# Performance work log

Hardware: AMD Instinct MI355X
Metric: run time of the kernel (lower is better)

The kernel has to match this reference:

```python
import jax, jax.numpy as jnp
import numpy as np

N, E, DIN, D, FE, L, B, M = 10000, 40000, 11, 64, 4, 4, 512, 3


def setup_inputs() -> dict:
    key = jax.random.key(0)
    ks = iter(jax.random.split(key, 24))
    s = lambda *sh: jax.random.normal(next(ks), sh, jnp.float32)
    return {
        "x": s(N, DIN),
        "edge_index": jax.random.randint(next(ks), (2, E), 0, N),
        "edge_attr": jax.random.uniform(next(ks), (E, FE), jnp.float32),
        "batch": jnp.sort(jax.random.randint(next(ks), (N,), 0, B)),
        "W0": s(DIN, D) * 0.1, "b0": jnp.zeros((D,), jnp.float32),
        "Wn1": s(FE, 2 * D) * 0.1, "bn1": jnp.zeros((2 * D,), jnp.float32),
        "Wn2": s(2 * D, D * D) * 0.02, "bn2": jnp.zeros((D * D,), jnp.float32),
        "root": s(L, D, D) * 0.1, "conv_bias": jnp.zeros((L, D), jnp.float32),
        "lstm_Wih": s(4 * D, 2 * D) * 0.1, "lstm_Whh": s(4 * D, D) * 0.1,
        "lstm_b": jnp.zeros((4 * D,), jnp.float32),
        "Wo1": s(2 * D, D) * 0.1, "bo1": jnp.zeros((D,), jnp.float32),
        "Wo2": s(D, 1) * 0.1, "bo2": jnp.zeros((1,), jnp.float32),
    }


def reference(x, edge_index, edge_attr, batch, W0, b0, Wn1, bn1, Wn2, bn2,
              root, conv_bias, lstm_Wih, lstm_Whh, lstm_b, Wo1, bo1, Wo2, bo2):
    src, dst = edge_index[0], edge_index[1]
    h = x @ W0 + b0  # [N, D]
    # Edge MLP is SHARED across all conv layers -> compute per-edge weight matrices once
    ew = (jax.nn.silu(edge_attr @ Wn1 + bn1) @ Wn2 + bn2).reshape(E, D, D)
    for l in range(L):
        msg = jnp.einsum('ed,edf->ef', h[src], ew)  # gather-compute per edge
        aggr = jax.ops.segment_sum(msg, dst, num_segments=N)  # scatter-add to targets
        h = h + (aggr + h @ root[l] + conv_bias[l])  # NNConv + residual
    # Set2Set pooling (LSTM, M processing steps)
    q_star = jnp.zeros((B, 2 * D), h.dtype)
    hs = jnp.zeros((B, D), h.dtype)
    cs = jnp.zeros((B, D), h.dtype)
    for _ in range(M):
        gates = q_star @ lstm_Wih.T + hs @ lstm_Whh.T + lstm_b
        i, f, g, o = jnp.split(gates, 4, axis=-1)  # torch LSTM gate order
        cs = jax.nn.sigmoid(f) * cs + jax.nn.sigmoid(i) * jnp.tanh(g)
        hs = jax.nn.sigmoid(o) * jnp.tanh(cs)
        q = hs  # [B, D]
        e = jnp.sum(h * q[batch], axis=-1)  # [N]
        emax = jax.ops.segment_max(e, batch, num_segments=B)
        ex = jnp.exp(e - emax[batch])
        denom = jax.ops.segment_sum(ex, batch, num_segments=B)
        a = ex / denom[batch]  # per-graph softmax attention
        r = jax.ops.segment_sum(a[:, None] * h, batch, num_segments=B)
        q_star = jnp.concatenate([q, r], axis=-1)
    out = jax.nn.silu(q_star @ Wo1 + bo1) @ Wo2 + bo2
    return out.reshape(-1)
```

## Files before the change

kernel.cpp:

```cpp
#include <hip/hip_runtime.h>
#include <cstdint>
#include <cstddef>

#define NN   10000
#define EE   40000
#define DIN_ 11
#define DD   64
#define LL   4
#define BB   512
#define MM   3
#define K1   128
#define DD2  4096
#define NPB  16
#define NCH  8
#define CSPL 2
#define CPB  4
#define ESLOT 12
#define ECREG (8 * ESLOT)

typedef unsigned short ushort_t;
typedef unsigned int   uint_t;

typedef __bf16 bf16x8_t __attribute__((ext_vector_type(8)));
typedef float  f32x4_t  __attribute__((ext_vector_type(4)));
union FragU { uint4 u; bf16x8_t b; };

__device__ __forceinline__ float bfu(ushort_t u) { return __uint_as_float(((uint_t)u) << 16); }
__device__ __forceinline__ float bflo(uint_t u) { return __uint_as_float(u << 16); }
__device__ __forceinline__ float bfhi(uint_t u) { return __uint_as_float(u & 0xffff0000u); }
__device__ __forceinline__ ushort_t f2bf(float f) {
  uint_t u = __float_as_uint(f);
  u = (u + 0x7fffu + ((u >> 16) & 1u)) >> 16;
  return (ushort_t)u;
}
__device__ __forceinline__ uint_t pack2(float lo, float hi) {
  return (uint_t)f2bf(lo) | ((uint_t)f2bf(hi) << 16);
}
__device__ __forceinline__ float sigmf_(float x) { return 1.f / (1.f + expf(-x)); }
__device__ __forceinline__ float siluf_(float x) { return x / (1.f + expf(-x)); }

#if defined(__HIP_DEVICE_COMPILE__) && __has_builtin(__builtin_amdgcn_fdot2_f32_bf16)
typedef __bf16 bf16x2_t __attribute__((ext_vector_type(2)));
__device__ __forceinline__ float dot2a(uint_t a, uint_t b, float c) {
  union { uint_t u; bf16x2_t v; } ua, ub;
  ua.u = a; ub.u = b;
  return __builtin_amdgcn_fdot2_f32_bf16(ua.v, ub.v, c, false);
}
#else
__device__ __forceinline__ float dot2a(uint_t a, uint_t b, float c) {
  return c + bflo(a) * bflo(b) + bfhi(a) * bfhi(b);
}
#endif

#define NCANON 16
struct CanonArgs {
  const void* src[NCANON];
  float* dst[NCANON];
  int n[NCANON];
};
__global__ void k_canon(CanonArgs a, const ushort_t* __restrict__ ea, int* __restrict__ flag) {
  __shared__ int bad;
  if (threadIdx.x == 0) bad = 0;
  __syncthreads();
  ushort_t u = ea[threadIdx.x];
  if ((u & 0x8000u) || u > 0x3F80u) atomicAdd(&bad, 1);
  __syncthreads();
  const int isbf = (bad == 0) ? 1 : 0;
  if (blockIdx.x == 0 && blockIdx.y == 0 && threadIdx.x == 0) *flag = isbf;
  const int ai = blockIdx.y;
  const int n = a.n[ai];
  const int i = blockIdx.x * 256 + threadIdx.x;
  if (i >= n) return;
  float v;
  if (isbf) v = bfu(((const ushort_t*)a.src[ai])[i]);
  else      v = ((const float*)a.src[ai])[i];
  a.dst[ai][i] = v;
}

__global__ void k_wn2m(const void* __restrict__ Wn2, uint_t* __restrict__ out,
                       const int* __restrict__ flag) {
  __shared__ ushort_t row[DD2];
  const int k = blockIdx.x, tid = threadIdx.x;
  if (*flag) {
    const uint4* src = (const uint4*)((const ushort_t*)Wn2 + (size_t)k * DD2);
    ((uint4*)row)[tid] = src[tid];
    ((uint4*)row)[tid + 256] = src[tid + 256];
  } else {
    const float* src = (const float*)Wn2 + (size_t)k * DD2;
    for (int j = 0; j < 16; ++j) row[tid + 256 * j] = f2bf(src[tid + 256 * j]);
  }
  __syncthreads();
  const int kpg = k >> 1, par = k & 1;
  const int lane = tid >> 2, jp = tid & 3;
  const int q = lane >> 4, n = lane & 15;
  for (int fc = 0; fc < 4; ++fc) {
#pragma unroll
    for (int hf = 0; hf < 2; ++hf) {
      int d0 = hf * 32 + q * 8 + 2 * jp;
      int f = fc * 16 + n;
      uint_t lo = row[d0 * 64 + f], hi = row[(d0 + 1) * 64 + f];
      out[((((size_t)kpg * 4 + fc) * 2 + par) * 2 + hf) * 256 + tid] = lo | (hi << 16);
    }
  }
}

__global__ void k_wT(const float* __restrict__ Wihc, const float* __restrict__ Whhc,
                     float* __restrict__ Wiht, float* __restrict__ Whht) {
  int idx = blockIdx.x * 256 + threadIdx.x;
  if (idx < 4 * DD * K1) {
    int j = idx >> 7, i = idx & 127;
    Wiht[i * 256 + j] = Wihc[idx];
  }
  if (idx < 4 * DD * DD) {
    int j = idx >> 6, i = idx & 63;
    Whht[i * 256 + j] = Whhc[idx];
  }
}

__global__ void k_embed(const float* __restrict__ x, const float* __restrict__ W0,
                        const float* __restrict__ b0, const float* __restrict__ bn2,
                        float* __restrict__ h, uint_t* __restrict__ hpk,
                        float* __restrict__ nbias) {
  __shared__ float xs[DIN_];
  __shared__ float hl[DD];
  const int n = blockIdx.x, f = threadIdx.x;
  if (f < DIN_) xs[f] = x[n * DIN_ + f];
  __syncthreads();
  float a = b0[f];
  for (int i = 0; i < DIN_; ++i) a += xs[i] * W0[i * DD + f];
  h[(size_t)n * DD + f] = a;
  hl[f] = a;
  float other = __shfl_down(a, 1);
  if ((f & 1) == 0)
    hpk[(size_t)n * 32 + (f >> 1)] = pack2(a, other);
  __syncthreads();
  float nb = 0.f;
#pragma unroll
  for (int d = 0; d < DD; ++d) nb += hl[d] * bn2[d * DD + f];
  nbias[(size_t)n * DD + f] = nb;
}

__global__ void k_edgemlp(const float* __restrict__ ea, const float* __restrict__ Wn1,
                          const float* __restrict__ bn1, const int* __restrict__ epos,
                          uint_t* __restrict__ hn1c) {
  int idx = blockIdx.x * 256 + threadIdx.x;
  if (idx >= EE * (K1 / 2)) return;
  int e = idx >> 6, j = idx & 63;
  int k0 = 2 * j, k1 = 2 * j + 1;
  float a0 = ea[e * 4 + 0], a1 = ea[e * 4 + 1], a2 = ea[e * 4 + 2], a3 = ea[e * 4 + 3];
  float t0 = bn1[k0] + a0 * Wn1[k0] + a1 * Wn1[K1 + k0] + a2 * Wn1[2 * K1 + k0] + a3 * Wn1[3 * K1 + k0];
  float t1 = bn1[k1] + a0 * Wn1[k1] + a1 * Wn1[K1 + k1] + a2 * Wn1[2 * K1 + k1] + a3 * Wn1[3 * K1 + k1];
  int pos = epos[e];
  hn1c[((size_t)(j >> 3) * EE + pos) * 8 + (j & 7)] = pack2(siluf_(t0), siluf_(t1));
}

__global__ void k_hist(const int* __restrict__ ei, int* __restrict__ cnt_s) {
  int e = blockIdx.x * 256 + threadIdx.x;
  if (e >= EE) return;
  atomicAdd(&cnt_s[ei[e]], 1);
}

__global__ void k_scan(const int* __restrict__ cnt, int* __restrict__ rp,
                       const int* __restrict__ batch, int* __restrict__ goff) {
  if (blockIdx.x == 1) {
    int g = threadIdx.x;
    if (g > BB) return;
    int lo = 0, hi = NN;
    while (lo < hi) {
      int mid = (lo + hi) >> 1;
      if (batch[mid] < g) lo = mid + 1; else hi = mid;
    }
    goff[g] = lo;
    return;
  }
  __shared__ int part[1024];
  const int tid = threadIdx.x;
  const int chunk = (NN + 1023) / 1024;
  int s = 0;
  for (int j = 0; j < chunk; ++j) {
    int idx = tid * chunk + j;
    if (idx < NN) s += cnt[idx];
  }
  part[tid] = s;
  __syncthreads();
  for (int off = 1; off < 1024; off <<= 1) {
    int v = (tid >= off) ? part[tid - off] : 0;
    __syncthreads();
    part[tid] += v;
    __syncthreads();
  }
  int base = (tid == 0) ? 0 : part[tid - 1];
  for (int j = 0; j < chunk; ++j) {
    int idx = tid * chunk + j;
    if (idx < NN) { rp[idx] = base; base += cnt[idx]; }
  }
  if (tid == 1023) rp[NN] = part[1023];
}

__global__ void k_fill(const int* __restrict__ ei, const int* __restrict__ rps,
                       int* __restrict__ cur_s, int* __restrict__ epos,
                       int* __restrict__ esd) {
  int e = blockIdx.x * 256 + threadIdx.x;
  if (e >= EE) return;
  int s = ei[e], d = ei[EE + e];
  int ps = atomicAdd(&cur_s[s], 1);
  int pos = rps[s] + ps;
  epos[e] = pos;
  esd[2 * pos] = s;
  esd[2 * pos + 1] = d;
}

__global__ __launch_bounds__(512, 4) void k_conv(
    const uint_t* __restrict__ hpk, const uint_t* __restrict__ hn1c,
    const uint_t* __restrict__ Wn2m, const float* __restrict__ nbias,
    const int* __restrict__ rps, const int* __restrict__ esd,
    float* __restrict__ aggr) {
  __shared__ uint_t Gp[NPB * 2 * 64 * 4];
  __shared__ int2 eStage[ECREG];
  const int tid = threadIdx.x;
  const int w = tid >> 6, lane = tid & 63;
  const int q = lane >> 4, n16 = lane & 15;
  const int half = blockIdx.x / 625;
  const int ng = blockIdx.x - half * 625;
  const int n0 = ng * NPB;
  const int e0 = rps[n0], e1 = rps[n0 + NPB];
  const int ecnt = e1 - e0;

  if (tid < ECREG && tid < ecnt) eStage[tid] = ((const int2*)esd)[e0 + tid];

  FragU a0, a1;
  {
    const uint4* ap = (const uint4*)(hpk + (size_t)(n0 + n16) * 32);
    a0.u = ap[q];
    a1.u = ap[4 + q];
  }
  __syncthreads();

  float acc[ESLOT];
#pragma unroll
  for (int s = 0; s < ESLOT; ++s) {
    const int li = w + 8 * s;
    float v = 0.f;
    if (half == 0 && li < ecnt && li < ECREG)
      v = nbias[(size_t)eStage[li].x * 64 + lane];
    acc[s] = v;
  }

  const int kq = w >> 2, slot = w & 3;
  for (int cc = 0; cc < CPB; ++cc) {
    const int c = half * CPB + cc;
    if (cc) __syncthreads();
    const int kpg = c * 8 + w;
    for (int fc = 0; fc < 4; ++fc) {
      const uint4* bp = (const uint4*)Wn2m + (size_t)(kpg * 4 + fc) * 256 + lane;
      FragU b00, b01, b10, b11;
      b00.u = bp[0];
      b01.u = bp[64];
      b10.u = bp[128];
      b11.u = bp[192];
      f32x4_t acc0 = {0.f, 0.f, 0.f, 0.f};
      f32x4_t acc1 = {0.f, 0.f, 0.f, 0.f};
      acc0 = __builtin_amdgcn_mfma_f32_16x16x32_bf16(a0.b, b00.b, acc0, 0, 0, 0);
      acc0 = __builtin_amdgcn_mfma_f32_16x16x32_bf16(a1.b, b01.b, acc0, 0, 0, 0);
      acc1 = __builtin_amdgcn_mfma_f32_16x16x32_bf16(a0.b, b10.b, acc1, 0, 0, 0);
      acc1 = __builtin_amdgcn_mfma_f32_16x16x32_bf16(a1.b, b11.b, acc1, 0, 0, 0);
#pragma unroll
      for (int r = 0; r < 4; ++r) {
        const int m = q * 4 + r;
        Gp[(((m * 2 + kq) * 64 + fc * 16 + n16) * 4 + slot)] = pack2(acc0[r], acc1[r]);
      }
    }
    __syncthreads();
#pragma unroll
    for (int s = 0; s < ESLOT; ++s) {
      const int li = w + 8 * s;
      if (li < ecnt && li < ECREG) {
        const int2 sd = eStage[li];
        const int m = sd.x - n0;
        const uint4* hp = (const uint4*)(hn1c + ((size_t)c * EE + e0 + li) * 8);
        uint4 hv0 = hp[0], hv1 = hp[1];
        const uint4* gb = (const uint4*)Gp + (size_t)(m * 2) * 64 + lane;
        uint4 g0 = gb[0], g1 = gb[64];
        float p = acc[s];
        p = dot2a(g0.x, hv0.x, p);
        p = dot2a(g0.y, hv0.y, p);
        p = dot2a(g0.z, hv0.z, p);
        p = dot2a(g0.w, hv0.w, p);
        p = dot2a(g1.x, hv1.x, p);
        p = dot2a(g1.y, hv1.y, p);
        p = dot2a(g1.z, hv1.z, p);
        p = dot2a(g1.w, hv1.w, p);
        acc[s] = p;
      }
    }
    for (int li = ECREG + w; li < ecnt; li += 8) {
      const int ii = e0 + li;
      const int src = __builtin_amdgcn_readfirstlane(esd[2 * ii]);
      const int dst = __builtin_amdgcn_readfirstlane(esd[2 * ii + 1]);
      const int m = src - n0;
      float p = (half == 0 && cc == 0) ? nbias[(size_t)src * 64 + lane] : 0.f;
      const uint4* hp = (const uint4*)(hn1c + ((size_t)c * EE + ii) * 8);
      uint4 hv0 = hp[0], hv1 = hp[1];
      const uint4* gb = (const uint4*)Gp + (size_t)(m * 2) * 64 + lane;
      uint4 g0 = gb[0], g1 = gb[64];
      p = dot2a(g0.x, hv0.x, p);
      p = dot2a(g0.y, hv0.y, p);
      p = dot2a(g0.z, hv0.z, p);
      p = dot2a(g0.w, hv0.w, p);
      p = dot2a(g1.x, hv1.x, p);
      p = dot2a(g1.y, hv1.y, p);
      p = dot2a(g1.z, hv1.z, p);
      p = dot2a(g1.w, hv1.w, p);
      atomicAdd(&aggr[(size_t)dst * 64 + lane], p);
    }
  }
#pragma unroll
  for (int s = 0; s < ESLOT; ++s) {
    const int li = w + 8 * s;
    if (li < ecnt && li < ECREG) {
      const int dst = eStage[li].y;
      atomicAdd(&aggr[(size_t)dst * 64 + lane], acc[s]);
    }
  }
}

__global__ __launch_bounds__(256) void k_update(
    float* __restrict__ h, uint_t* __restrict__ hpk,
    float* __restrict__ aggr, const float* __restrict__ bn2,
    const float* __restrict__ root, const float* __restrict__ cb,
    float* __restrict__ nbias, int l) {
  __shared__ float hl[4][DD];
  __shared__ float al[4][DD];
  const int tid = threadIdx.x, w = tid >> 6, f = tid & 63;
  const int n = blockIdx.x * 4 + w;
  float hv = h[(size_t)n * DD + f];
  hl[w][f] = hv;
  float acc = hv + aggr[(size_t)n * DD + f] + cb[l * DD + f];
  aggr[(size_t)n * DD + f] = 0.f;
  __syncthreads();
  const float* rp = root + (size_t)l * DD2;
#pragma unroll
  for (int d = 0; d < DD; ++d) acc += hl[w][d] * rp[d * DD + f];
  h[(size_t)n * DD + f] = acc;
  al[w][f] = acc;
  float other = __shfl_down(acc, 1);
  if ((f & 1) == 0)
    hpk[(size_t)n * 32 + (f >> 1)] = pack2(acc, other);
  __syncthreads();
  float nb = 0.f;
#pragma unroll
  for (int d = 0; d < DD; ++d) nb += al[w][d] * bn2[d * DD + f];
  nbias[(size_t)n * DD + f] = nb;
}

#define EVCAP 2048
__global__ void k_s2s(const float* __restrict__ h, const int* __restrict__ goff,
                      const float* __restrict__ Wiht, const float* __restrict__ Whht,
                      const float* __restrict__ lb,
                      const float* __restrict__ Wo1, const float* __restrict__ bo1,
                      const float* __restrict__ Wo2, const float* __restrict__ bo2,
                      void* __restrict__ outv, const int* __restrict__ flag) {
  __shared__ float qsl[K1];
  __shared__ float hsl[DD];
  __shared__ float csl[DD];
  __shared__ float gl[4][DD];
  __shared__ float red[256];
  __shared__ float ev[EVCAP];
  __shared__ float rp4[4][DD];
  const int g = blockIdx.x, tid = threadIdx.x;

  if (tid < K1) qsl[tid] = 0.f;
  else if (tid < K1 + DD) hsl[tid - K1] = 0.f;
  else csl[tid - K1 - DD] = 0.f;
  __syncthreads();

  const int i0 = goff[g];
  int cnt = goff[g + 1] - i0;
  if (cnt > EVCAP) cnt = EVCAP;

  for (int m = 0; m < MM; ++m) {
    {
      float a = lb[tid];
      for (int i = 0; i < K1; ++i) a += qsl[i] * Wiht[i * 256 + tid];
      for (int i = 0; i < DD; ++i) a += hsl[i] * Whht[i * 256 + tid];
      gl[tid >> 6][tid & 63] = a;
    }
    __syncthreads();
    if (tid < DD) {
      float ig = sigmf_(gl[0][tid]), fg = sigmf_(gl[1][tid]);
      float gg = tanhf(gl[2][tid]), og = sigmf_(gl[3][tid]);
      float c = fg * csl[tid] + ig * gg;
      csl[tid] = c;
      hsl[tid] = og * tanhf(c);
    }
    __syncthreads();
    float lmax = -1e30f;
    for (int jj = tid; jj < cnt; jj += 256) {
      const float* hp = h + (size_t)(i0 + jj) * DD;
      float e = 0.f;
#pragma unroll
      for (int d = 0; d < DD; ++d) e += hp[d] * hsl[d];
      ev[jj] = e;
      lmax = fmaxf(lmax, e);
    }
    red[tid] = lmax;
    __syncthreads();
    for (int s = 128; s > 0; s >>= 1) {
      if (tid < s) red[tid] = fmaxf(red[tid], red[tid + s]);
      __syncthreads();
    }
    const float emax = red[0];
    __syncthreads();
    float lsum = 0.f;
    for (int jj = tid; jj < cnt; jj += 256) {
      float ex = expf(ev[jj] - emax);
      ev[jj] = ex;
      lsum += ex;
    }
    red[tid] = lsum;
    __syncthreads();
    for (int s = 128; s > 0; s >>= 1) {
      if (tid < s) red[tid] += red[tid + s];
      __syncthreads();
    }
    const float denom = red[0];
    const int f = tid & 63, grp = tid >> 6;
    float acc = 0.f;
    for (int jj = grp; jj < cnt; jj += 4)
      acc += ev[jj] * h[(size_t)(i0 + jj) * DD + f];
    rp4[grp][f] = acc;
    __syncthreads();
    if (tid < DD) {
      float r = rp4[0][tid] + rp4[1][tid] + rp4[2][tid] + rp4[3][tid];
      r = (cnt > 0 && denom > 0.f) ? r / denom : 0.f;
      qsl[tid] = hsl[tid];
      qsl[DD + tid] = r;
    }
    __syncthreads();
  }
  if (tid < DD) {
    float t = bo1[tid];
    for (int i = 0; i < K1; ++i) t += qsl[i] * Wo1[i * DD + tid];
    float s = siluf_(t) * Wo2[tid];
    for (int off = 32; off > 0; off >>= 1) s += __shfl_down(s, off);
    if (tid == 0) {
      float v = s + bo2[0];
      if (*flag) ((ushort_t*)outv)[g] = f2bf(v);
      else       ((float*)outv)[g] = v;
    }
  }
}

extern "C" void kernel_launch(void* const* d_in, const int* in_sizes, int n_in,
                              void* d_out, int out_size, void* d_ws, size_t ws_size,
                              hipStream_t stream) {
  const void* x_r    = d_in[0];
  const int*  ei     = (const int*)d_in[1];
  const void* ea_r   = d_in[2];
  const int*  batch  = (const int*)d_in[3];
  const void* W0_r   = d_in[4];
  const void* b0_r   = d_in[5];
  const void* Wn1_r  = d_in[6];
  const void* bn1_r  = d_in[7];
  const void* Wn2_r  = d_in[8];
  const void* bn2_r  = d_in[9];
  const void* root_r = d_in[10];
  const void* cb_r   = d_in[11];
  const void* Wih_r  = d_in[12];
  const void* Whh_r  = d_in[13];
  const void* lb_r   = d_in[14];
  const void* Wo1_r  = d_in[15];
  const void* bo1_r  = d_in[16];
  const void* Wo2_r  = d_in[17];
  const void* bo2_r  = d_in[18];

  char* w = (char*)d_ws;
  size_t off = 0;
  auto alloc = [&](size_t bytes) -> void* {
    void* p = w + off;
    off = (off + bytes + 255) & ~(size_t)255;
    return p;
  };
  int* flag = (int*)alloc(4);
  float* xc    = (float*)alloc((size_t)NN * DIN_ * 4);
  float* eac   = (float*)alloc((size_t)EE * 4 * 4);
  float* W0c   = (float*)alloc((size_t)DIN_ * DD * 4);
  float* b0c   = (float*)alloc((size_t)DD * 4);
  float* Wn1c  = (float*)alloc((size_t)4 * K1 * 4);
  float* bn1c  = (float*)alloc((size_t)K1 * 4);
  float* bn2c  = (float*)alloc((size_t)DD2 * 4);
  float* rootc = (float*)alloc((size_t)LL * DD2 * 4);
  float* cbc   = (float*)alloc((size_t)LL * DD * 4);
  float* Wihc  = (float*)alloc((size_t)4 * DD * K1 * 4);
  float* Whhc  = (float*)alloc((size_t)4 * DD * DD * 4);
  float* lbc   = (float*)alloc((size_t)4 * DD * 4);
  float* Wo1c  = (float*)alloc((size_t)K1 * DD * 4);
  float* bo1c  = (float*)alloc((size_t)DD * 4);
  float* Wo2c  = (float*)alloc((size_t)DD * 4);
  float* bo2c  = (float*)alloc((size_t)4);
  float* Wiht  = (float*)alloc((size_t)K1 * 256 * 4);
  float* Whht  = (float*)alloc((size_t)DD * 256 * 4);
  uint_t* Wn2m = (uint_t*)alloc((size_t)64 * 4 * 2 * 2 * 64 * 4 * 4);
  float*  h    = (float*)alloc((size_t)NN * DD * 4);
  uint_t* hpk  = (uint_t*)alloc((size_t)NN * 32 * 4);
  uint_t* hn1c = (uint_t*)alloc((size_t)EE * (K1 / 2) * 4);
  float*  aggr = (float*)alloc((size_t)NN * DD * 4);
  float*  nbias= (float*)alloc((size_t)NN * DD * 4);
  int* cnts  = (int*)alloc((size_t)2 * NN * 4);
  int* rps   = (int*)alloc((size_t)(NN + 1) * 4);
  int* epos  = (int*)alloc((size_t)EE * 4);
  int* esd   = (int*)alloc((size_t)2 * EE * 4);
  int* goff  = (int*)alloc((size_t)(BB + 1) * 4);

  int* cnt_s = cnts;
  int* cur_s = cnts + NN;

  hipMemsetAsync(cnts, 0, (size_t)2 * NN * 4, stream);
  hipMemsetAsync(aggr, 0, (size_t)NN * DD * 4, stream);

  CanonArgs ca;
  const void* srcs[NCANON] = {x_r, ea_r, W0_r, b0_r, Wn1_r, bn1_r, bn2_r, root_r,
                              cb_r, Wih_r, Whh_r, lb_r, Wo1_r, bo1_r, Wo2_r, bo2_r};
  float* dsts[NCANON] = {xc, eac, W0c, b0c, Wn1c, bn1c, bn2c, rootc,
                         cbc, Wihc, Whhc, lbc, Wo1c, bo1c, Wo2c, bo2c};
  int cnts_c[NCANON] = {NN * DIN_, EE * 4, DIN_ * DD, DD, 4 * K1, K1, DD2, LL * DD2,
                        LL * DD, 4 * DD * K1, 4 * DD * DD, 4 * DD, K1 * DD, DD, DD, 1};
  for (int i = 0; i < NCANON; ++i) { ca.src[i] = srcs[i]; ca.dst[i] = dsts[i]; ca.n[i] = cnts_c[i]; }
  {
    dim3 grid((EE * 4 + 255) / 256, NCANON);
    k_canon<<<grid, 256, 0, stream>>>(ca, (const ushort_t*)ea_r, flag);
  }
  k_wn2m<<<K1, 256, 0, stream>>>(Wn2_r, Wn2m, flag);
  k_wT<<<(4 * DD * K1 + 255) / 256, 256, 0, stream>>>(Wihc, Whhc, Wiht, Whht);

  k_embed<<<NN, DD, 0, stream>>>(xc, W0c, b0c, bn2c, h, hpk, nbias);
  k_hist<<<(EE + 255) / 256, 256, 0, stream>>>(ei, cnt_s);
  k_scan<<<2, 1024, 0, stream>>>(cnt_s, rps, batch, goff);
  k_fill<<<(EE + 255) / 256, 256, 0, stream>>>(ei, rps, cur_s, epos, esd);
  k_edgemlp<<<(EE * (K1 / 2) + 255) / 256, 256, 0, stream>>>(eac, Wn1c, bn1c, epos, hn1c);

  for (int l = 0; l < LL; ++l) {
    k_conv<<<CSPL * (NN / NPB), 512, 0, stream>>>(hpk, hn1c, Wn2m, nbias, rps, esd, aggr);
    k_update<<<NN / 4, 256, 0, stream>>>(h, hpk, aggr, bn2c, rootc, cbc, nbias, l);
  }

  k_s2s<<<BB, 256, 0, stream>>>(h, goff, Wiht, Whht, lbc, Wo1c, bo1c, Wo2c, bo2c,
                                d_out, flag);
}
```

Measured before the change: 458.7 us.

## Stage per-edge hidden vectors in LDS and vectorize Gp stores in conv kernel

At kernel start, the per-edge hn1c rows for all four channel chunks are loaded cooperatively into a new LDS buffer. The per-edge inner loop then reads them from LDS rather than issuing repeated global loads. The MFMA loop is remapped so each wave handles one fc column across four slots, which lets it pack the results and write Gp as 16-byte vector stores instead of scalar stores. This adds about 12KB of LDS per block, which may lower occupancy under launch_bounds(512,4).

```diff
diff --git a/kernel.cpp b/kernel.cpp
--- a/kernel.cpp
+++ b/kernel.cpp
@@ -17,6 +17,7 @@
 #define CPB  4
 #define ESLOT 12
 #define ECREG (8 * ESLOT)
+#define EHW (ECREG * 8)
 
 typedef unsigned short ushort_t;
 typedef unsigned int   uint_t;
@@ -215,7 +216,8 @@
     const uint_t* __restrict__ Wn2m, const float* __restrict__ nbias,
     const int* __restrict__ rps, const int* __restrict__ esd,
     float* __restrict__ aggr) {
-  __shared__ uint_t Gp[NPB * 2 * 64 * 4];
+  __shared__ __align__(16) uint_t Gp[NPB * 2 * 64 * 4];
+  __shared__ __align__(16) uint_t eh[CPB * EHW];
   __shared__ int2 eStage[ECREG];
   const int tid = threadIdx.x;
   const int w = tid >> 6, lane = tid & 63;
@@ -225,8 +227,19 @@
   const int n0 = ng * NPB;
   const int e0 = rps[n0], e1 = rps[n0 + NPB];
   const int ecnt = e1 - e0;
+  const int ecap = ecnt < ECREG ? ecnt : ECREG;
 
   if (tid < ECREG && tid < ecnt) eStage[tid] = ((const int2*)esd)[e0 + tid];
+
+  uint4 st0, st1, st2, st3;
+  const bool stv = (tid < ecap * 2);
+  if (stv) {
+    const size_t base = ((size_t)(half * CPB) * EE + e0) * 8;
+    st0 = ((const uint4*)(hn1c + base))[tid];
+    st1 = ((const uint4*)(hn1c + base + (size_t)EE * 8))[tid];
+    st2 = ((const uint4*)(hn1c + base + (size_t)2 * EE * 8))[tid];
+    st3 = ((const uint4*)(hn1c + base + (size_t)3 * EE * 8))[tid];
+  }
 
   FragU a0, a1;
   {
@@ -241,18 +254,27 @@
   for (int s = 0; s < ESLOT; ++s) {
     const int li = w + 8 * s;
     float v = 0.f;
-    if (half == 0 && li < ecnt && li < ECREG)
+    if (half == 0 && li < ecap)
       v = nbias[(size_t)eStage[li].x * 64 + lane];
     acc[s] = v;
   }
 
-  const int kq = w >> 2, slot = w & 3;
+  if (stv) {
+    ((uint4*)(eh + 0 * EHW))[tid] = st0;
+    ((uint4*)(eh + 1 * EHW))[tid] = st1;
+    ((uint4*)(eh + 2 * EHW))[tid] = st2;
+    ((uint4*)(eh + 3 * EHW))[tid] = st3;
+  }
+
+  const int kq = w >> 2, fcw = w & 3;
   for (int cc = 0; cc < CPB; ++cc) {
     const int c = half * CPB + cc;
     if (cc) __syncthreads();
-    const int kpg = c * 8 + w;
-    for (int fc = 0; fc < 4; ++fc) {
-      const uint4* bp = (const uint4*)Wn2m + (size_t)(kpg * 4 + fc) * 256 + lane;
+    uint_t pk[4][4];
+#pragma unroll
+    for (int slot = 0; slot < 4; ++slot) {
+      const int kpg = c * 8 + kq * 4 + slot;
+      const uint4* bp = (const uint4*)Wn2m + (size_t)(kpg * 4 + fcw) * 256 + lane;
       FragU b00, b01, b10, b11;
       b00.u = bp[0];
       b01.u = bp[64];
@@ -265,20 +287,24 @@
       acc1 = __builtin_amdgcn_mfma_f32_16x16x32_bf16(a0.b, b10.b, acc1, 0, 0, 0);
       acc1 = __builtin_amdgcn_mfma_f32_16x16x32_bf16(a1.b, b11.b, acc1, 0, 0, 0);
 #pragma unroll
-      for (int r = 0; r < 4; ++r) {
-        const int m = q * 4 + r;
-        Gp[(((m * 2 + kq) * 64 + fc * 16 + n16) * 4 + slot)] = pack2(acc0[r], acc1[r]);
-      }
-    }
-    __syncthreads();
+      for (int r = 0; r < 4; ++r) pk[r][slot] = pack2(acc0[r], acc1[r]);
+    }
+#pragma unroll
+    for (int r = 0; r < 4; ++r) {
+      const int m = q * 4 + r;
+      uint4 v;
+      v.x = pk[r][0]; v.y = pk[r][1]; v.z = pk[r][2]; v.w = pk[r][3];
+      ((uint4*)Gp)[(size_t)(m * 2 + kq) * 64 + fcw * 16 + n16] = v;
+    }
+    __syncthreads();
+    const uint4* ehb = (const uint4*)(eh + cc * EHW);
 #pragma unroll
     for (int s = 0; s < ESLOT; ++s) {
       const int li = w + 8 * s;
-      if (li < ecnt && li < ECREG) {
+      if (li < ecap) {
         const int2 sd = eStage[li];
         const int m = sd.x - n0;
-        const uint4* hp = (const uint4*)(hn1c + ((size_t)c * EE + e0 + li) * 8);
-        uint4 hv0 = hp[0], hv1 = hp[1];
+        uint4 hv0 = ehb[li * 2], hv1 = ehb[li * 2 + 1];
         const uint4* gb = (const uint4*)Gp + (size_t)(m * 2) * 64 + lane;
         uint4 g0 = gb[0], g1 = gb[64];
         float p = acc[s];
@@ -317,7 +343,7 @@
 #pragma unroll
   for (int s = 0; s < ESLOT; ++s) {
     const int li = w + 8 * s;
-    if (li < ecnt && li < ECREG) {
+    if (li < ecap) {
       const int dst = eStage[li].y;
       atomicAdd(&aggr[(size_t)dst * 64 + lane], acc[s]);
     }
```

New measurement: 404.5 us. -11.8%, faster.
